# Performance work log

Hardware: AMD Instinct MI355X
Metric: run time of the kernel (lower is better)

The kernel has to match this reference:

```python
import jax, jax.numpy as jnp
import numpy as np
from jax import lax


def _instance_loss(z1, z2, t):
    # z1, z2: [B,T,C]; t: [B,T] timestamps
    B, T, C = z1.shape
    if B == 1:
        return jnp.asarray(0.0, z1.dtype)
    N = B * T
    tf = t.reshape(N)
    diff = jnp.abs(tf[:, None] - tf[None, :])          # [N,N]
    seq = jnp.repeat(jnp.arange(B), T)                 # sequence id per row
    same_seq = seq[:, None] == seq[None, :]
    diff = jnp.where(same_seq, diff + diff.max() + 0.001, diff)
    # k=B smallest diffs per row (cross-sequence temporal neighbors)
    _, idx = lax.top_k(-diff, B)                       # [N,B]
    z1f = z1.reshape(N, C)
    z2f = z2.reshape(N, C)
    pos = jnp.sum(z1f * z2f, axis=-1)[:, None]         # [N,1]
    neg1 = jnp.einsum('nc,nkc->nk', z1f, z1f[idx])     # [N,B]
    neg2 = jnp.einsum('nc,nkc->nk', z1f, z2f[idx])     # [N,B]
    logits = jnp.concatenate([pos, neg1, neg2], axis=1)
    return -jax.nn.log_softmax(logits, axis=1)[:, 0].mean()


def _temporal_loss(z1, z2):
    B, T, C = z1.shape
    if T == 1:
        return jnp.asarray(0.0, z1.dtype)
    z = jnp.concatenate([z1, z2], axis=1)              # [B,2T,C]
    n = 2 * T
    sim = jnp.einsum('bic,bjc->bij', z, z)             # [B,2T,2T]
    # tril(sim,-1)[:,:,:-1] + triu(sim,1)[:,:,1:] == drop-diagonal shift
    i = jnp.arange(n)[:, None]
    j = jnp.arange(n - 1)[None, :]
    logits = jnp.where(j < i, sim[:, :, : n - 1], sim[:, :, 1:])  # [B,2T,2T-1]
    nls = -jax.nn.log_softmax(logits, axis=-1)
    tt = jnp.arange(T)
    return (nls[:, tt, T + tt - 1].mean() + nls[:, T + tt, tt].mean()) / 2


def _max_pool2(z):
    # F.max_pool1d(kernel=2, stride=2) over time axis (floor, drops odd tail)
    B, T, C = z.shape
    T2 = T // 2
    return z[:, : 2 * T2].reshape(B, T2, 2, C).max(axis=2)


def hierarchical_contrastive_loss(z1, z2, t, alpha=0.5, temporal_unit=0):
    B = z1.shape[0]
    loss = jnp.asarray(0.0, z1.dtype)
    d = 0
    while z1.shape[1] > 1:
        if alpha != 0:
            loss = loss + alpha * _instance_loss(z1, z2, t)
        if d >= temporal_unit and (1 - alpha) != 0:
            loss = loss + (1 - alpha) * _temporal_loss(z1, z2)
        d += 1
        z1 = _max_pool2(z1)
        z2 = _max_pool2(z2)
        Tt = t.shape[1]
        if Tt % 2 != 0:
            t = t[:, :-1]
        t = t.reshape(B, -1, 2).mean(axis=2)
    if z1.shape[1] == 1:
        if alpha != 0:
            loss = loss + alpha * _instance_loss(z1, z2, t)
        d += 1
    return loss / d


def setup_inputs() -> dict:
    key = jax.random.key(0)
    k1, k2, k3 = jax.random.split(key, 3)
    B, T, C = 8, 512, 320
    z1 = jax.random.normal(k1, (B, T, C), dtype=jnp.float32)
    z2 = jax.random.normal(k2, (B, T, C), dtype=jnp.float32)
    # irregular, increasing timestamps per sequence
    t = jnp.sort(jax.random.uniform(k3, (B, T), dtype=jnp.float32) * T, axis=1)
    return {"z1": z1, "z2": z2, "t": t}


def reference(z1, z2, t):
    return hierarchical_contrastive_loss(z1, z2, t, alpha=0.5, temporal_unit=0)
```

## Files before the change

kernel.cpp:

```cpp
#include <hip/hip_runtime.h>
#include <math.h>

#define BB 8
#define CC 320
#define ZB 2618880
#define TTOT 4088
#define NROWS 8184
#define NROWS_T 16352
#define NTBLK 440
#define NP1V 81920
#define NP2 5120
#define NMRB 64

#define FT 2618880
#define FPART 2622968
#define FCROSS 2799032
#define FROW 2807208
#define FBLK 2815396
#define FCNT 2815460

constexpr int kT[10]       = {512,256,128,64,32,16,8,4,2,1};
constexpr int kLogT[10]    = {9,8,7,6,5,4,3,2,1,0};
constexpr int kZBoff[10]   = {0,1310720,1966080,2293760,2457600,2539520,2580480,2600960,2611200,2616320};
constexpr int kToff[10]    = {0,0,2048,3072,3584,3840,3968,4032,4064,4080};
constexpr int kRowcum[11]  = {0,4096,6144,7168,7680,7936,8064,8128,8160,8176,8184};
constexpr int kTRowcum[10] = {0,8192,12288,14336,15360,15872,16128,16256,16320,16352};
constexpr int kNt128[9]    = {8,4,2,1,1,1,1,1,1};
constexpr int kLog128[9]   = {3,2,1,0,0,0,0,0,0};
constexpr int kPoff128[9]  = {0,65536,81920,86016,87040,87552,87808,87936,88000};
constexpr int kSblkcum[10] = {0,288,368,392,400,408,416,424,432,440};
constexpr int kXoff[9]     = {0,4096,6144,7168,7680,7936,8064,8128,8160};

typedef short v8s __attribute__((ext_vector_type(8)));
typedef float v16f __attribute__((ext_vector_type(16)));

__device__ __forceinline__ unsigned short f2bf(float x) {
    unsigned int u = __float_as_uint(x);
    u = (u + 0x7FFFu + ((u >> 16) & 1u)) >> 16;
    return (unsigned short)u;
}
__device__ __forceinline__ float bfu(unsigned short u) {
    return __uint_as_float(((unsigned int)u) << 16);
}
__device__ __forceinline__ float4 fmax4(float4 a, float4 b) {
    return make_float4(fmaxf(a.x, b.x), fmaxf(a.y, b.y), fmaxf(a.z, b.z),
                       fmaxf(a.w, b.w));
}
__device__ __forceinline__ ushort4 bf4(float4 v) {
    return make_ushort4(f2bf(v.x), f2bf(v.y), f2bf(v.z), f2bf(v.w));
}

__global__ void pool03_kernel(const float* __restrict__ z1,
                              const float* __restrict__ z2,
                              const float* __restrict__ t,
                              unsigned short* __restrict__ zb,
                              float* __restrict__ tpool,
                              int* __restrict__ counter) {
    int gid = blockIdx.x * 256 + threadIdx.x;
    if (gid == 0) *counter = 0;
    if (gid < NP1V) {
        int c4 = (gid % 80) * 4;
        int rest = gid / 80;
        int ch = rest & 63;
        int b = (rest >> 6) & 7;
        int which = rest >> 9;
        const float* src =
            (which ? z2 : z1) + ((size_t)(b * 512 + ch * 8)) * CC + c4;
        unsigned short* dst = zb + (size_t)which * ZB;
        float4 v[8];
#pragma unroll
        for (int j = 0; j < 8; j++)
            v[j] = *(const float4*)(src + (size_t)j * CC);
#pragma unroll
        for (int j = 0; j < 8; j++)
            *(ushort4*)(dst + (size_t)(b * 512 + ch * 8 + j) * CC + c4) =
                bf4(v[j]);
        float4 m1[4];
#pragma unroll
        for (int j = 0; j < 4; j++) m1[j] = fmax4(v[2 * j], v[2 * j + 1]);
#pragma unroll
        for (int j = 0; j < 4; j++)
            *(ushort4*)(dst + kZBoff[1] +
                        (size_t)(b * 256 + ch * 4 + j) * CC + c4) = bf4(m1[j]);
        float4 m2[2] = {fmax4(m1[0], m1[1]), fmax4(m1[2], m1[3])};
#pragma unroll
        for (int j = 0; j < 2; j++)
            *(ushort4*)(dst + kZBoff[2] +
                        (size_t)(b * 128 + ch * 2 + j) * CC + c4) = bf4(m2[j]);
        *(ushort4*)(dst + kZBoff[3] + (size_t)(b * 64 + ch) * CC + c4) =
            bf4(fmax4(m2[0], m2[1]));
    } else if (gid < NP1V + TTOT) {
        int i = gid - NP1V;
        int l = 1;
#pragma unroll
        for (int q = 2; q <= 9; q++) l = (i >= kToff[q]) ? q : l;
        int rem = i - kToff[l];
        int Tl = kT[l];
        int t2 = rem & (Tl - 1);
        int b = rem >> kLogT[l];
        int win = 512 / Tl;
        const float* p = t + b * 512 + t2 * win;
        float s = 0.f;
        for (int j = 0; j < win; j++) s += p[j];
        tpool[kToff[l] + rem] = s * (1.0f / win);
    }
}

__global__ void pool49_kernel(unsigned short* __restrict__ zb) {
    int gid = blockIdx.x * 256 + threadIdx.x;
    if (gid >= NP2) return;
    int c = gid % CC;
    int r2 = gid / CC;
    int b = r2 & 7;
    int which = r2 >> 3;
    unsigned short* base = zb + (size_t)which * ZB;
    const unsigned short* src = base + kZBoff[3] + (size_t)(b * 64) * CC + c;
    float a[32];
#pragma unroll
    for (int j = 0; j < 32; j++)
        a[j] = fmaxf(bfu(src[(size_t)(2 * j) * CC]),
                     bfu(src[(size_t)(2 * j + 1) * CC]));
#pragma unroll
    for (int j = 0; j < 32; j++)
        base[kZBoff[4] + (size_t)(b * 32 + j) * CC + c] = f2bf(a[j]);
#pragma unroll
    for (int j = 0; j < 16; j++) a[j] = fmaxf(a[2 * j], a[2 * j + 1]);
#pragma unroll
    for (int j = 0; j < 16; j++)
        base[kZBoff[5] + (size_t)(b * 16 + j) * CC + c] = f2bf(a[j]);
#pragma unroll
    for (int j = 0; j < 8; j++) a[j] = fmaxf(a[2 * j], a[2 * j + 1]);
#pragma unroll
    for (int j = 0; j < 8; j++)
        base[kZBoff[6] + (size_t)(b * 8 + j) * CC + c] = f2bf(a[j]);
#pragma unroll
    for (int j = 0; j < 4; j++) a[j] = fmaxf(a[2 * j], a[2 * j + 1]);
#pragma unroll
    for (int j = 0; j < 4; j++)
        base[kZBoff[7] + (size_t)(b * 4 + j) * CC + c] = f2bf(a[j]);
#pragma unroll
    for (int j = 0; j < 2; j++) a[j] = fmaxf(a[2 * j], a[2 * j + 1]);
#pragma unroll
    for (int j = 0; j < 2; j++)
        base[kZBoff[8] + (size_t)(b * 2 + j) * CC + c] = f2bf(a[j]);
    base[kZBoff[9] + (size_t)b * CC + c] = f2bf(fmaxf(a[0], a[1]));
}

__global__ void topk_kernel(const unsigned short* __restrict__ zb,
                            const float* __restrict__ t0,
                            const float* __restrict__ tpool,
                            float* __restrict__ rowloss) {
    int wave = threadIdx.x >> 6, lane = threadIdx.x & 63;
    int row = blockIdx.x * 4 + wave;
    if (row >= NROWS) return;
    int l = 0;
#pragma unroll
    for (int q = 1; q <= 9; q++) l = (row >= kRowcum[q]) ? q : l;
    int n = row - kRowcum[l];
    int T = kT[l];
    const float* tt = l ? tpool + kToff[l] : t0;
    int seq = n >> kLogT[l];
    float tn = tt[n];

    int idx8[8];
    {
        int s = lane >> 3, j = lane & 7;
        const float* ts = tt + s * T;
        bool own = (s == seq);
        int lo = 0, hi = T;
        while (lo < hi) {
            int mid = (lo + hi) >> 1;
            if (ts[mid] < tn) lo = mid + 1; else hi = mid;
        }
        int ilo = lo - 1 - j, ihi = lo + j;
        unsigned long long ka, kb;
        if (own) {
            ka = (j == 0) ? (((unsigned long long)__float_as_uint(1.0e12f)
                              << 32) | (unsigned int)n)
                          : ~0ULL;
            kb = ~0ULL;
        } else {
            ka = (ilo >= 0)
                     ? (((unsigned long long)__float_as_uint(tn - ts[ilo])
                         << 32) | (unsigned int)(s * T + ilo))
                     : ~0ULL;
            kb = (ihi < T)
                     ? (((unsigned long long)__float_as_uint(ts[ihi] - tn)
                         << 32) | (unsigned int)(s * T + ihi))
                     : ~0ULL;
        }
#pragma unroll
        for (int r = 0; r < 8; r++) {
            unsigned long long k = (ka < kb) ? ka : kb;
            unsigned long long o;
            o = __shfl_xor(k, 1);  k = (k < o) ? k : o;
            o = __shfl_xor(k, 2);  k = (k < o) ? k : o;
            o = __shfl_xor(k, 4);  k = (k < o) ? k : o;
            o = __shfl_xor(k, 8);  k = (k < o) ? k : o;
            o = __shfl_xor(k, 16); k = (k < o) ? k : o;
            o = __shfl_xor(k, 32); k = (k < o) ? k : o;
            idx8[r] = (int)(unsigned int)(k & 0xffffffffull);
            if (ka == k) ka = ~0ULL;
            else if (kb == k) kb = ~0ULL;
        }
    }

    const unsigned short* z1 = zb + kZBoff[l];
    const unsigned short* z2 = zb + ZB + kZBoff[l];
    const unsigned short* z1n = z1 + (size_t)n * CC;
    const unsigned short* z2n = z2 + (size_t)n * CC;
    float a[5];
#pragma unroll
    for (int j = 0; j < 5; j++) a[j] = bfu(z1n[lane + 64 * j]);
    float part[17];
    {
        float s = 0.f;
#pragma unroll
        for (int j = 0; j < 5; j++) s += a[j] * bfu(z2n[lane + 64 * j]);
        part[0] = s;
    }
#pragma unroll
    for (int k = 0; k < 8; k++) {
        int p = idx8[k];
        const unsigned short* r1 = z1 + (size_t)p * CC;
        const unsigned short* r2 = z2 + (size_t)p * CC;
        float s1 = 0.f, s2 = 0.f;
#pragma unroll
        for (int j = 0; j < 5; j++) {
            float av = a[j];
            s1 += av * bfu(r1[lane + 64 * j]);
            s2 += av * bfu(r2[lane + 64 * j]);
        }
        part[1 + k] = s1;
        part[9 + k] = s2;
    }
#pragma unroll
    for (int q = 0; q < 17; q++) {
        float v = part[q];
        for (int off = 32; off > 0; off >>= 1) v += __shfl_xor(v, off);
        part[q] = v;
    }
    if (lane == 0) {
        float m = part[0];
#pragma unroll
        for (int q = 1; q < 17; q++) m = fmaxf(m, part[q]);
        float s = 0.f;
#pragma unroll
        for (int q = 0; q < 17; q++) s += expf(part[q] - m);
        float w = 0.05f / (float)(BB * T);
        rowloss[row] = w * (m + logf(s) - part[0]);
    }
}

__global__ void __launch_bounds__(256) temporal_kernel(
        const unsigned short* __restrict__ zb, float2* __restrict__ part,
        float* __restrict__ crossbuf) {
    __shared__ __align__(16) char smem[16512];
    int bid = blockIdx.x, tid = threadIdx.x;
    int l = 0;
#pragma unroll
    for (int q = 1; q <= 8; q++) l = (bid >= kSblkcum[q]) ? q : l;
    int rem = bid - kSblkcum[l];
    int b = rem & 7;
    int pr = rem >> 3;
    int Tl = kT[l], n = 2 * Tl, lnt = kLog128[l];
    int rt = 0, width = kNt128[l];
    while (pr >= width) { pr -= width; rt++; width--; }
    int ct = rt + pr;
    bool diag = (rt == ct);
    const unsigned short* zb1 = zb + kZBoff[l] + (size_t)b * Tl * CC;
    const unsigned short* zb2 = zb + ZB + kZBoff[l] + (size_t)b * Tl * CC;
    int row0 = rt * 128, col0 = ct * 128;
    int w = tid >> 6, lane = tid & 63;
    unsigned short* As = (unsigned short*)smem;
    unsigned short* Bs = (unsigned short*)(smem + 8192);
    float2* cred = (float2*)smem;

    v16f acc[4];
#pragma unroll
    for (int cs = 0; cs < 4; cs++)
#pragma unroll
        for (int e = 0; e < 16; e++) acc[cs][e] = 0.f;

    int sofq[2]; const unsigned short* srcA[2]; const unsigned short* srcB[2];
    bool vA[2], vB[2];
#pragma unroll
    for (int q = 0; q < 2; q++) {
        int g = q * 256 + tid;
        int r = g & 127, kbb = g >> 7;
        sofq[q] = (r >> 5) * 1024 + (kbb >> 1) * 512 + (kbb & 1) * 256 +
                  (r & 31) * 8;
        int ka = kbb * 8;
        int gr = row0 + r;
        vA[q] = gr < n;
        srcA[q] = vA[q] ? ((gr < Tl) ? zb1 + (size_t)gr * CC + ka
                                     : zb2 + (size_t)(gr - Tl) * CC + ka)
                        : zb1;
        int gc = col0 + r;
        vB[q] = gc < n;
        srcB[q] = vB[q] ? ((gc < Tl) ? zb1 + (size_t)gc * CC + ka
                                     : zb2 + (size_t)(gc - Tl) * CC + ka)
                        : zb1;
    }

    for (int kc = 0; kc < CC; kc += 32) {
#pragma unroll
        for (int q = 0; q < 2; q++) {
            uint4 av = vA[q] ? *(const uint4*)(srcA[q] + kc)
                             : make_uint4(0, 0, 0, 0);
            *(uint4*)(As + sofq[q]) = av;
            if (!diag) {
                uint4 bv = vB[q] ? *(const uint4*)(srcB[q] + kc)
                                 : make_uint4(0, 0, 0, 0);
                *(uint4*)(Bs + sofq[q]) = bv;
            }
        }
        __syncthreads();
        const unsigned short* Ab = As + w * 1024;
        const unsigned short* Bb = diag ? As : Bs;
#pragma unroll
        for (int cc = 0; cc < 2; cc++) {
            v8s af = *(const v8s*)(Ab + cc * 512 + lane * 8);
#pragma unroll
            for (int cs = 0; cs < 4; cs++) {
                v8s bf = *(const v8s*)(Bb + cs * 1024 + cc * 512 + lane * 8);
                acc[cs] = __builtin_amdgcn_mfma_f32_32x32x16_bf16(
                    af, bf, acc[cs], 0, 0, 0);
            }
        }
        __syncthreads();
    }

    int colin = lane & 31;
    int rowhalf = 4 * (lane >> 5);

#pragma unroll
    for (int r = 0; r < 16; r++) {
        int lrow = (r & 3) + 8 * (r >> 2) + rowhalf;
        int grow = row0 + w * 32 + lrow;
        float vals[4];
        float lm = -3.0e38f;
#pragma unroll
        for (int cs = 0; cs < 4; cs++) {
            int gcol = col0 + cs * 32 + colin;
            float v = acc[cs][r];
            if (gcol >= n || gcol == grow) v = -3.0e38f;
            vals[cs] = v;
            lm = fmaxf(lm, v);
        }
#pragma unroll
        for (int off = 1; off < 32; off <<= 1)
            lm = fmaxf(lm, __shfl_xor(lm, off));
        float ls = 0.f;
#pragma unroll
        for (int cs = 0; cs < 4; cs++)
            ls += (vals[cs] > -1.0e38f) ? expf(vals[cs] - lm) : 0.f;
#pragma unroll
        for (int off = 1; off < 32; off <<= 1) ls += __shfl_xor(ls, off);
        if (colin == 0 && grow < n)
            part[kPoff128[l] + ((b * n + grow) << lnt) + ct] =
                make_float2(lm, ls);
    }

    if (ct - rt == (Tl >> 7)) {
#pragma unroll
        for (int r = 0; r < 16; r++) {
            int lrow = (r & 3) + 8 * (r >> 2) + rowhalf;
            int grow = row0 + w * 32 + lrow;
            if (grow < Tl) {
                int cidx = grow + Tl - col0;
                int cs_p = cidx >> 5, colin_p = cidx & 31;
                float cand = 0.f;
#pragma unroll
                for (int cs = 0; cs < 4; cs++)
                    cand += (cs == cs_p && colin == colin_p) ? acc[cs][r] : 0.f;
#pragma unroll
                for (int off = 1; off < 32; off <<= 1)
                    cand += __shfl_xor(cand, off);
                if (colin == 0)
                    crossbuf[kXoff[l] + b * Tl + grow] = cand;
            }
        }
    }

    if (!diag) {
#pragma unroll
        for (int cs = 0; cs < 4; cs++) {
            float m = acc[cs][0];
#pragma unroll
            for (int r = 1; r < 16; r++) m = fmaxf(m, acc[cs][r]);
            float mo = __shfl_xor(m, 32);
            float mm = fmaxf(m, mo);
            float s = 0.f;
#pragma unroll
            for (int r = 0; r < 16; r++) s += expf(acc[cs][r] - mm);
            s += __shfl_xor(s, 32);
            if (lane < 32) cred[w * 128 + cs * 32 + lane] = make_float2(mm, s);
        }
    }
    __syncthreads();
    if (!diag && tid < 128) {
        float2 a0 = cred[0 * 128 + tid], a1 = cred[1 * 128 + tid];
        float2 a2 = cred[2 * 128 + tid], a3 = cred[3 * 128 + tid];
        float M = fmaxf(fmaxf(a0.x, a1.x), fmaxf(a2.x, a3.x));
        float S = a0.y * expf(a0.x - M) + a1.y * expf(a1.x - M) +
                  a2.y * expf(a2.x - M) + a3.y * expf(a3.x - M);
        int gcol = col0 + tid;
        part[kPoff128[l] + ((b * n + gcol) << lnt) + rt] = make_float2(M, S);
    }
}

__device__ __forceinline__ void d_merge_row(
        int row, const float2* __restrict__ part,
        const float* __restrict__ crossbuf, float* local) {
    int l = 0;
#pragma unroll
    for (int q = 1; q <= 8; q++) l = (row >= kTRowcum[q]) ? q : l;
    int r = row - kTRowcum[l];
    int Tl = kT[l], n = 2 * Tl, nt = kNt128[l], lnt = kLog128[l];
    int b = r >> (kLogT[l] + 1);
    int rr = r & (n - 1);
    const float2* p = part + kPoff128[l] + ((size_t)(b * n + rr) << lnt);
    float M = -3.0e38f, S = 0.f;
    for (int k = 0; k < nt; k++) {
        float2 q2 = p[k];
        float nM = fmaxf(M, q2.x);
        S = S * expf(M - nM) + q2.y * expf(q2.x - nM);
        M = nM;
    }
    float cross = crossbuf[kXoff[l] + b * Tl + (rr < Tl ? rr : rr - Tl)];
    float w = 0.025f / (float)(BB * Tl);
    *local += w * (M + logf(S) - cross);
}

__global__ void merge_reduce_kernel(const float2* __restrict__ part,
                                    const float* __restrict__ crossbuf,
                                    const float* __restrict__ rowloss,
                                    float* __restrict__ blockpart,
                                    int* __restrict__ counter,
                                    float* __restrict__ out) {
    __shared__ float redsm[4];
    __shared__ int flag;
    int bid = blockIdx.x, tid = threadIdx.x;
    int gid = bid * 256 + tid;
    int wave = tid >> 6, lane = tid & 63;
    float local = 0.f;
    if (gid < NROWS_T) d_merge_row(gid, part, crossbuf, &local);
    if (gid < NROWS) local += rowloss[gid];
#pragma unroll
    for (int off = 32; off > 0; off >>= 1) local += __shfl_xor(local, off);
    if (lane == 0) redsm[wave] = local;
    __syncthreads();
    if (tid == 0) {
        float bs = redsm[0] + redsm[1] + redsm[2] + redsm[3];
        atomicExch(blockpart + bid, bs);
        __threadfence();
        int old = atomicAdd(counter, 1);
        flag = (old == NMRB - 1) ? 1 : 0;
    }
    __syncthreads();
    if (flag && tid < 64) {
        float v = atomicAdd(blockpart + tid, 0.0f);
#pragma unroll
        for (int off = 32; off > 0; off >>= 1) v += __shfl_xor(v, off);
        if (tid == 0) out[0] = v;
    }
}

extern "C" void kernel_launch(void* const* d_in, const int* in_sizes, int n_in,
                              void* d_out, int out_size, void* d_ws,
                              size_t ws_size, hipStream_t stream) {
    const float* z1 = (const float*)d_in[0];
    const float* z2 = (const float*)d_in[1];
    const float* t  = (const float*)d_in[2];
    float* ws = (float*)d_ws;
    unsigned short* zb = (unsigned short*)ws;
    float* tpool = ws + FT;
    float2* part = (float2*)(ws + FPART);
    float* crossbuf = ws + FCROSS;
    float* rowloss = ws + FROW;
    float* blockpart = ws + FBLK;
    int* counter = (int*)(ws + FCNT);
    float* out = (float*)d_out;

    pool03_kernel<<<(NP1V + TTOT + 255) / 256, 256, 0, stream>>>(
        z1, z2, t, zb, tpool, counter);
    pool49_kernel<<<(NP2 + 255) / 256, 256, 0, stream>>>(zb);
    topk_kernel<<<NROWS / 4, 256, 0, stream>>>(zb, t, tpool, rowloss);
    temporal_kernel<<<NTBLK, 256, 0, stream>>>(zb, part, crossbuf);
    merge_reduce_kernel<<<NMRB, 256, 0, stream>>>(part, crossbuf, rowloss,
                                                  blockpart, counter, out);
}
```

Before: 108.0 us.

## Fold pool49 and merge-reduce kernels into neighbors via atomic counter spin-waits

Drops the launch count from five to three. The deep pooling levels (4-9) and a serial timestamp cascade now run in the first blocks of the top-k kernel, and top-k rows at coarse levels spin on an atomic counter until those blocks finish. The final merge/reduce runs in extra blocks appended to the temporal kernel, which spin until all temporal blocks have signalled. This removes launch gaps but relies on the producer blocks being scheduled ahead of the waiting ones. It also adds a serial per-sequence cascade and busy-wait traffic.

```diff
diff --git a/kernel.cpp b/kernel.cpp
--- a/kernel.cpp
+++ b/kernel.cpp
@@ -4,13 +4,14 @@
 #define BB 8
 #define CC 320
 #define ZB 2618880
-#define TTOT 4088
 #define NROWS 8184
 #define NROWS_T 16352
 #define NTBLK 440
+#define NMRB 64
 #define NP1V 81920
+#define NT1 2048
 #define NP2 5120
-#define NMRB 64
+#define NPB 20
 
 #define FT 2618880
 #define FPART 2622968
@@ -55,9 +56,9 @@
                               const float* __restrict__ t,
                               unsigned short* __restrict__ zb,
                               float* __restrict__ tpool,
-                              int* __restrict__ counter) {
+                              int* __restrict__ cnt) {
     int gid = blockIdx.x * 256 + threadIdx.x;
-    if (gid == 0) *counter = 0;
+    if (gid < 3) cnt[gid] = 0;
     if (gid < NP1V) {
         int c4 = (gid % 80) * 4;
         int rest = gid / 80;
@@ -89,26 +90,16 @@
                         (size_t)(b * 128 + ch * 2 + j) * CC + c4) = bf4(m2[j]);
         *(ushort4*)(dst + kZBoff[3] + (size_t)(b * 64 + ch) * CC + c4) =
             bf4(fmax4(m2[0], m2[1]));
-    } else if (gid < NP1V + TTOT) {
+    } else if (gid < NP1V + NT1) {
         int i = gid - NP1V;
-        int l = 1;
-#pragma unroll
-        for (int q = 2; q <= 9; q++) l = (i >= kToff[q]) ? q : l;
-        int rem = i - kToff[l];
-        int Tl = kT[l];
-        int t2 = rem & (Tl - 1);
-        int b = rem >> kLogT[l];
-        int win = 512 / Tl;
-        const float* p = t + b * 512 + t2 * win;
-        float s = 0.f;
-        for (int j = 0; j < win; j++) s += p[j];
-        tpool[kToff[l] + rem] = s * (1.0f / win);
-    }
-}
-
-__global__ void pool49_kernel(unsigned short* __restrict__ zb) {
-    int gid = blockIdx.x * 256 + threadIdx.x;
-    if (gid >= NP2) return;
+        int b = i >> 8, j = i & 255;
+        tpool[b * 256 + j] =
+            0.5f * (t[b * 512 + 2 * j] + t[b * 512 + 2 * j + 1]);
+    }
+}
+
+__device__ __forceinline__ void d_pool49_item(int gid,
+                                              unsigned short* __restrict__ zb) {
     int c = gid % CC;
     int r2 = gid / CC;
     int b = r2 & 7;
@@ -146,18 +137,76 @@
     base[kZBoff[9] + (size_t)b * CC + c] = f2bf(fmaxf(a[0], a[1]));
 }
 
-__global__ void topk_kernel(const unsigned short* __restrict__ zb,
+__device__ __forceinline__ void d_tcascade(int b, float* __restrict__ tpool) {
+    const float* l1 = tpool + b * 256;
+    float a3 = 0.f, a4 = 0.f, a5 = 0.f, a6 = 0.f, a7 = 0.f, a8 = 0.f,
+          a9 = 0.f;
+    for (int g = 0; g < 128; g++) {
+        float m = 0.5f * (l1[2 * g] + l1[2 * g + 1]);
+        tpool[kToff[2] + b * 128 + g] = m;
+        a3 = (g & 1) ? 0.5f * (a3 + m) : m;
+        if (g & 1) {
+            int j3 = g >> 1;
+            tpool[kToff[3] + b * 64 + j3] = a3;
+            a4 = (j3 & 1) ? 0.5f * (a4 + a3) : a3;
+            if (j3 & 1) {
+                int j4 = j3 >> 1;
+                tpool[kToff[4] + b * 32 + j4] = a4;
+                a5 = (j4 & 1) ? 0.5f * (a5 + a4) : a4;
+                if (j4 & 1) {
+                    int j5 = j4 >> 1;
+                    tpool[kToff[5] + b * 16 + j5] = a5;
+                    a6 = (j5 & 1) ? 0.5f * (a6 + a5) : a5;
+                    if (j5 & 1) {
+                        int j6 = j5 >> 1;
+                        tpool[kToff[6] + b * 8 + j6] = a6;
+                        a7 = (j6 & 1) ? 0.5f * (a7 + a6) : a6;
+                        if (j6 & 1) {
+                            int j7 = j6 >> 1;
+                            tpool[kToff[7] + b * 4 + j7] = a7;
+                            a8 = (j7 & 1) ? 0.5f * (a8 + a7) : a7;
+                            if (j7 & 1) {
+                                int j8 = j7 >> 1;
+                                tpool[kToff[8] + b * 2 + j8] = a8;
+                                a9 = (j8 & 1) ? 0.5f * (a9 + a8) : a8;
+                                if (j8 & 1) tpool[kToff[9] + b] = a9;
+                            }
+                        }
+                    }
+                }
+            }
+        }
+    }
+}
+
+__global__ void topk_kernel(unsigned short* __restrict__ zb,
                             const float* __restrict__ t0,
-                            const float* __restrict__ tpool,
-                            float* __restrict__ rowloss) {
-    int wave = threadIdx.x >> 6, lane = threadIdx.x & 63;
-    int row = blockIdx.x * 4 + wave;
+                            float* __restrict__ tpool,
+                            float* __restrict__ rowloss,
+                            int* __restrict__ cnt) {
+    int bid = blockIdx.x, tid = threadIdx.x;
+    if (bid < NPB) {
+        int gid = bid * 256 + tid;
+        if (gid < NP2) d_pool49_item(gid, zb);
+        if (bid == 0 && tid < 8) d_tcascade(tid, tpool);
+        __syncthreads();
+        __threadfence();
+        if (tid == 0) atomicAdd(cnt + 0, 1);
+        return;
+    }
+    int wave = tid >> 6, lane = tid & 63;
+    int row = (bid - NPB) * 4 + wave;
     if (row >= NROWS) return;
     int l = 0;
 #pragma unroll
     for (int q = 1; q <= 9; q++) l = (row >= kRowcum[q]) ? q : l;
     int n = row - kRowcum[l];
     int T = kT[l];
+    if (row >= 6144) {
+        if (lane == 0)
+            while (atomicAdd(cnt + 0, 0) < NPB) {}
+        __threadfence();
+    }
     const float* tt = l ? tpool + kToff[l] : t0;
     int seq = n >> kLogT[l];
     float tn = tt[n];
@@ -252,11 +301,72 @@
     }
 }
 
+__device__ __forceinline__ void d_merge_row(
+        int row, const float2* __restrict__ part,
+        const float* __restrict__ crossbuf, float* local) {
+    int l = 0;
+#pragma unroll
+    for (int q = 1; q <= 8; q++) l = (row >= kTRowcum[q]) ? q : l;
+    int r = row - kTRowcum[l];
+    int Tl = kT[l], n = 2 * Tl, nt = kNt128[l], lnt = kLog128[l];
+    int b = r >> (kLogT[l] + 1);
+    int rr = r & (n - 1);
+    const float2* p = part + kPoff128[l] + ((size_t)(b * n + rr) << lnt);
+    float M = -3.0e38f, S = 0.f;
+    for (int k = 0; k < nt; k++) {
+        float2 q2 = p[k];
+        float nM = fmaxf(M, q2.x);
+        S = S * expf(M - nM) + q2.y * expf(q2.x - nM);
+        M = nM;
+    }
+    float cross = crossbuf[kXoff[l] + b * Tl + (rr < Tl ? rr : rr - Tl)];
+    float w = 0.025f / (float)(BB * Tl);
+    *local += w * (M + logf(S) - cross);
+}
+
 __global__ void __launch_bounds__(256) temporal_kernel(
         const unsigned short* __restrict__ zb, float2* __restrict__ part,
-        float* __restrict__ crossbuf) {
+        float* __restrict__ crossbuf, const float* __restrict__ rowloss,
+        float* __restrict__ blockpart, int* __restrict__ cnt,
+        float* __restrict__ out) {
     __shared__ __align__(16) char smem[16512];
     int bid = blockIdx.x, tid = threadIdx.x;
+
+    if (bid >= NTBLK) {
+        __shared__ float redsm[4];
+        __shared__ int flag;
+        if (tid == 0)
+            while (atomicAdd(cnt + 1, 0) < NTBLK) {}
+        __syncthreads();
+        __threadfence();
+        int mb = bid - NTBLK;
+        int gid = mb * 256 + tid;
+        int wave = tid >> 6, lane = tid & 63;
+        float local = 0.f;
+        if (gid < NROWS_T) d_merge_row(gid, part, crossbuf, &local);
+        if (gid < NROWS) local += rowloss[gid];
+#pragma unroll
+        for (int off = 32; off > 0; off >>= 1)
+            local += __shfl_xor(local, off);
+        if (lane == 0) redsm[wave] = local;
+        __syncthreads();
+        if (tid == 0) {
+            float bs = redsm[0] + redsm[1] + redsm[2] + redsm[3];
+            atomicExch(blockpart + mb, bs);
+            __threadfence();
+            int old = atomicAdd(cnt + 2, 1);
+            flag = (old == NMRB - 1) ? 1 : 0;
+        }
+        __syncthreads();
+        if (flag && tid < 64) {
+            float v = atomicAdd(blockpart + tid, 0.0f);
+#pragma unroll
+            for (int off = 32; off > 0; off >>= 1) v += __shfl_xor(v, off);
+            if (tid == 0) out[0] = v;
+        }
+        return;
+    }
+
     int l = 0;
 #pragma unroll
     for (int q = 1; q <= 8; q++) l = (bid >= kSblkcum[q]) ? q : l;
@@ -408,62 +518,11 @@
         int gcol = col0 + tid;
         part[kPoff128[l] + ((b * n + gcol) << lnt) + rt] = make_float2(M, S);
     }
-}
-
-__device__ __forceinline__ void d_merge_row(
-        int row, const float2* __restrict__ part,
-        const float* __restrict__ crossbuf, float* local) {
-    int l = 0;
-#pragma unroll
-    for (int q = 1; q <= 8; q++) l = (row >= kTRowcum[q]) ? q : l;
-    int r = row - kTRowcum[l];
-    int Tl = kT[l], n = 2 * Tl, nt = kNt128[l], lnt = kLog128[l];
-    int b = r >> (kLogT[l] + 1);
-    int rr = r & (n - 1);
-    const float2* p = part + kPoff128[l] + ((size_t)(b * n + rr) << lnt);
-    float M = -3.0e38f, S = 0.f;
-    for (int k = 0; k < nt; k++) {
-        float2 q2 = p[k];
-        float nM = fmaxf(M, q2.x);
-        S = S * expf(M - nM) + q2.y * expf(q2.x - nM);
-        M = nM;
-    }
-    float cross = crossbuf[kXoff[l] + b * Tl + (rr < Tl ? rr : rr - Tl)];
-    float w = 0.025f / (float)(BB * Tl);
-    *local += w * (M + logf(S) - cross);
-}
-
-__global__ void merge_reduce_kernel(const float2* __restrict__ part,
-                                    const float* __restrict__ crossbuf,
-                                    const float* __restrict__ rowloss,
-                                    float* __restrict__ blockpart,
-                                    int* __restrict__ counter,
-                                    float* __restrict__ out) {
-    __shared__ float redsm[4];
-    __shared__ int flag;
-    int bid = blockIdx.x, tid = threadIdx.x;
-    int gid = bid * 256 + tid;
-    int wave = tid >> 6, lane = tid & 63;
-    float local = 0.f;
-    if (gid < NROWS_T) d_merge_row(gid, part, crossbuf, &local);
-    if (gid < NROWS) local += rowloss[gid];
-#pragma unroll
-    for (int off = 32; off > 0; off >>= 1) local += __shfl_xor(local, off);
-    if (lane == 0) redsm[wave] = local;
+
     __syncthreads();
     if (tid == 0) {
-        float bs = redsm[0] + redsm[1] + redsm[2] + redsm[3];
-        atomicExch(blockpart + bid, bs);
         __threadfence();
-        int old = atomicAdd(counter, 1);
-        flag = (old == NMRB - 1) ? 1 : 0;
-    }
-    __syncthreads();
-    if (flag && tid < 64) {
-        float v = atomicAdd(blockpart + tid, 0.0f);
-#pragma unroll
-        for (int off = 32; off > 0; off >>= 1) v += __shfl_xor(v, off);
-        if (tid == 0) out[0] = v;
+        atomicAdd(cnt + 1, 1);
     }
 }
 
@@ -480,14 +539,13 @@
     float* crossbuf = ws + FCROSS;
     float* rowloss = ws + FROW;
     float* blockpart = ws + FBLK;
-    int* counter = (int*)(ws + FCNT);
+    int* cnt = (int*)(ws + FCNT);
     float* out = (float*)d_out;
 
-    pool03_kernel<<<(NP1V + TTOT + 255) / 256, 256, 0, stream>>>(
-        z1, z2, t, zb, tpool, counter);
-    pool49_kernel<<<(NP2 + 255) / 256, 256, 0, stream>>>(zb);
-    topk_kernel<<<NROWS / 4, 256, 0, stream>>>(zb, t, tpool, rowloss);
-    temporal_kernel<<<NTBLK, 256, 0, stream>>>(zb, part, crossbuf);
-    merge_reduce_kernel<<<NMRB, 256, 0, stream>>>(part, crossbuf, rowloss,
-                                                  blockpart, counter, out);
-}
+    pool03_kernel<<<(NP1V + NT1 + 255) / 256, 256, 0, stream>>>(
+        z1, z2, t, zb, tpool, cnt);
+    topk_kernel<<<NPB + NROWS / 4, 256, 0, stream>>>(zb, t, tpool, rowloss,
+                                                     cnt);
+    temporal_kernel<<<NTBLK + NMRB, 256, 0, stream>>>(
+        zb, part, crossbuf, rowloss, blockpart, cnt, out);
+}
```

Result: slower. 144.8 us (+34.2%).
